# Kernel tuning notes

Measured on AMD Instinct MI355X. Metric: run time of the kernel, lower is better.

Reference implementation:

```python
import jax, jax.numpy as jnp
import numpy as np


def setup_inputs() -> dict:
    key = jax.random.key(0)
    k1, k2 = jax.random.split(key)
    B, D, K = 8192, 4096, 16
    x = jax.random.normal(k1, (B, D), dtype=jnp.float32)
    # kaiming_uniform_(a=sqrt(5)) on [K, D]: bound = sqrt(6/((1+5)*fan_in)) = 1/sqrt(D)
    bound = 1.0 / np.sqrt(D)
    w = jax.random.uniform(k2, (K, D), dtype=jnp.float32, minval=-bound, maxval=bound)
    return {"x": x, "w": w}


def reference(x, w):
    # z[b,d] = x[b,d] * (1 + sum_{i=1..k} w[i-1,d] * x[b,(d+i) mod D])
    k = w.shape[0]
    acc = jnp.ones_like(x)
    for i in range(1, k + 1):
        acc = acc + w[i - 1][None, :] * jnp.roll(x, -i, axis=1)
    return x * acc
```

## Files before the change

### kernel.cpp

```cpp
#include <hip/hip_runtime.h>


#define D 4096
#define DG 1024
#define K 16
#define TPB 256
#define TILE_B 8
#define ROW_F4 260
#define ROW_F (ROW_F4 * 4)

__global__ __launch_bounds__(TPB) void quad_enhancer_kernel(
    const float* __restrict__ x, const float* __restrict__ w,
    float* __restrict__ out) {
  __shared__ float lds[TILE_B * ROW_F];

  const int tid = threadIdx.x;
  const int cg0 = blockIdx.x * TPB;
  const int cg = cg0 + tid;
  const int b0 = blockIdx.y * TILE_B;

  const float4* x4 = (const float4*)x;

#pragma unroll
  for (int r = 0; r < TILE_B; ++r) {
    const float4* gptr = &x4[(size_t)(b0 + r) * DG + cg];
    float* lptr = &lds[r * ROW_F + tid * 4];
    __builtin_amdgcn_global_load_lds(
        (const __attribute__((address_space(1))) void*)gptr,
        (__attribute__((address_space(3))) void*)lptr, 16, 0, 0);
  }
  float4 halo;
  int hr = 0, hj = 0;
  if (tid < TILE_B * 4) {
    hr = tid >> 2;
    hj = tid & 3;
    halo = x4[(size_t)(b0 + hr) * DG + ((cg0 + 256 + hj) & (DG - 1))];
  }

  const float4* w4 = (const float4*)w;
  float4 wv[K];
#pragma unroll
  for (int i = 0; i < K; ++i) wv[i] = w4[i * DG + cg];

  if (tid < TILE_B * 4) {
    *(float4*)&lds[hr * ROW_F + (256 + hj) * 4] = halo;
  }
  __syncthreads();

  float4* out4 = (float4*)out;
#pragma unroll 2
  for (int r = 0; r < TILE_B; ++r) {
    const float4* lrow = (const float4*)&lds[r * ROW_F];
    float xs[20];
#pragma unroll
    for (int j = 0; j < 5; ++j) {
      float4 v = lrow[tid + j];
      xs[4 * j + 0] = v.x;
      xs[4 * j + 1] = v.y;
      xs[4 * j + 2] = v.z;
      xs[4 * j + 3] = v.w;
    }
    float ax = 1.0f, ay = 1.0f, az = 1.0f, aw = 1.0f;
#pragma unroll
    for (int i = 0; i < K; ++i) {
      ax = fmaf(wv[i].x, xs[i + 1], ax);
      ay = fmaf(wv[i].y, xs[i + 2], ay);
      az = fmaf(wv[i].z, xs[i + 3], az);
      aw = fmaf(wv[i].w, xs[i + 4], aw);
    }
    float4 o;
    o.x = xs[0] * ax;
    o.y = xs[1] * ay;
    o.z = xs[2] * az;
    o.w = xs[3] * aw;
    out4[(size_t)(b0 + r) * DG + cg] = o;
  }
}

extern "C" void kernel_launch(void* const* d_in, const int* in_sizes, int n_in,
                              void* d_out, int out_size, void* d_ws, size_t ws_size,
                              hipStream_t stream) {
  const float* x = (const float*)d_in[0];
  const float* w = (const float*)d_in[1];
  float* out = (float*)d_out;
  const int B = in_sizes[0] / D;

  dim3 grid(DG / TPB, B / TILE_B);
  quad_enhancer_kernel<<<grid, TPB, 0, stream>>>(x, w, out);
}
```

Baseline: 235.8 us.

## Replace LDS staging with direct register double-buffered global loads and nontemporal stores

Removes the shared-memory tile and barrier. Each thread now loads its own float4 plus the four neighbouring float4s straight from global memory, relying on the cache to serve the overlapping reads. Rows are processed in a two-buffer register pipeline over 16 rows per block, and outputs are written with nontemporal stores. This trades LDS traffic and synchronisation for five times as many global load instructions and more register pressure, and it halves the grid size.

```diff
diff --git a/kernel.cpp b/kernel.cpp
--- a/kernel.cpp
+++ b/kernel.cpp
@@ -5,60 +5,47 @@
 #define DG 1024
 #define K 16
 #define TPB 256
-#define TILE_B 8
-#define ROW_F4 260
-#define ROW_F (ROW_F4 * 4)
+#define RPB 16
+
+typedef float f32x4 __attribute__((ext_vector_type(4)));
 
 __global__ __launch_bounds__(TPB) void quad_enhancer_kernel(
     const float* __restrict__ x, const float* __restrict__ w,
     float* __restrict__ out) {
-  __shared__ float lds[TILE_B * ROW_F];
+  const int tid = threadIdx.x;
+  const int cg = blockIdx.x * TPB + tid;
+  const int b0 = blockIdx.y * RPB;
 
-  const int tid = threadIdx.x;
-  const int cg0 = blockIdx.x * TPB;
-  const int cg = cg0 + tid;
-  const int b0 = blockIdx.y * TILE_B;
+  const float4* __restrict__ x4 = (const float4*)x;
+  const float4* __restrict__ w4 = (const float4*)w;
+  f32x4* __restrict__ out4 = (f32x4*)out;
 
-  const float4* x4 = (const float4*)x;
+  const int g1 = (cg + 1) & (DG - 1);
+  const int g2 = (cg + 2) & (DG - 1);
+  const int g3 = (cg + 3) & (DG - 1);
+  const int g4 = (cg + 4) & (DG - 1);
 
-#pragma unroll
-  for (int r = 0; r < TILE_B; ++r) {
-    const float4* gptr = &x4[(size_t)(b0 + r) * DG + cg];
-    float* lptr = &lds[r * ROW_F + tid * 4];
-    __builtin_amdgcn_global_load_lds(
-        (const __attribute__((address_space(1))) void*)gptr,
-        (__attribute__((address_space(3))) void*)lptr, 16, 0, 0);
-  }
-  float4 halo;
-  int hr = 0, hj = 0;
-  if (tid < TILE_B * 4) {
-    hr = tid >> 2;
-    hj = tid & 3;
-    halo = x4[(size_t)(b0 + hr) * DG + ((cg0 + 256 + hj) & (DG - 1))];
-  }
-
-  const float4* w4 = (const float4*)w;
   float4 wv[K];
 #pragma unroll
   for (int i = 0; i < K; ++i) wv[i] = w4[i * DG + cg];
 
-  if (tid < TILE_B * 4) {
-    *(float4*)&lds[hr * ROW_F + (256 + hj) * 4] = halo;
-  }
-  __syncthreads();
+  auto loadrow = [&](int b, float4* buf) {
+    const float4* __restrict__ xr = x4 + (size_t)b * DG;
+    buf[0] = xr[cg];
+    buf[1] = xr[g1];
+    buf[2] = xr[g2];
+    buf[3] = xr[g3];
+    buf[4] = xr[g4];
+  };
 
-  float4* out4 = (float4*)out;
-#pragma unroll 2
-  for (int r = 0; r < TILE_B; ++r) {
-    const float4* lrow = (const float4*)&lds[r * ROW_F];
+  auto compute_store = [&](int b, const float4* buf) {
     float xs[20];
 #pragma unroll
     for (int j = 0; j < 5; ++j) {
-      float4 v = lrow[tid + j];
-      xs[4 * j + 0] = v.x;
-      xs[4 * j + 1] = v.y;
-      xs[4 * j + 2] = v.z;
-      xs[4 * j + 3] = v.w;
+      xs[4 * j + 0] = buf[j].x;
+      xs[4 * j + 1] = buf[j].y;
+      xs[4 * j + 2] = buf[j].z;
+      xs[4 * j + 3] = buf[j].w;
     }
     float ax = 1.0f, ay = 1.0f, az = 1.0f, aw = 1.0f;
 #pragma unroll
@@ -68,12 +55,22 @@
       az = fmaf(wv[i].z, xs[i + 3], az);
       aw = fmaf(wv[i].w, xs[i + 4], aw);
     }
-    float4 o;
+    f32x4 o;
     o.x = xs[0] * ax;
     o.y = xs[1] * ay;
     o.z = xs[2] * az;
     o.w = xs[3] * aw;
-    out4[(size_t)(b0 + r) * DG + cg] = o;
+    __builtin_nontemporal_store(o, &out4[(size_t)b * DG + cg]);
+  };
+
+  float4 bufA[5], bufB[5];
+  loadrow(b0, bufA);
+#pragma unroll 1
+  for (int r = 0; r < RPB; r += 2) {
+    loadrow(b0 + r + 1, bufB);
+    compute_store(b0 + r, bufA);
+    if (r + 2 < RPB) loadrow(b0 + r + 2, bufA);
+    compute_store(b0 + r + 1, bufB);
   }
 }
 
@@ -85,6 +82,6 @@
   float* out = (float*)d_out;
   const int B = in_sizes[0] / D;
 
-  dim3 grid(DG / TPB, B / TILE_B);
+  dim3 grid(DG / TPB, B / RPB);
   quad_enhancer_kernel<<<grid, TPB, 0, stream>>>(x, w, out);
 }
```

Result: slower. 256.4 us (+8.7%).

## Double-buffer LDS row tiles across a persistent row loop with nontemporal stores

Applied to the files above, without the earlier changes.

Each block now handles 32 rows as eight 4-row tiles. The next tile is loaded into a second LDS buffer with async global_load_lds while the current tile is computed, and w is loaded into registers once per block instead of once per 8 rows. Output uses nontemporal stores to reduce cache pollution. The trade-off is a grid four times smaller (1024 blocks), which leaves less parallelism for hiding latency, plus a per-tile barrier.

```diff
diff --git a/kernel.cpp b/kernel.cpp
--- a/kernel.cpp
+++ b/kernel.cpp
@@ -5,75 +5,103 @@
 #define DG 1024
 #define K 16
 #define TPB 256
-#define TILE_B 8
+#define TILE_B 4
+#define NT 8
 #define ROW_F4 260
 #define ROW_F (ROW_F4 * 4)
+#define BUF_F (TILE_B * ROW_F)
+
+typedef float f32x4 __attribute__((ext_vector_type(4)));
 
 __global__ __launch_bounds__(TPB) void quad_enhancer_kernel(
     const float* __restrict__ x, const float* __restrict__ w,
     float* __restrict__ out) {
-  __shared__ float lds[TILE_B * ROW_F];
+  __shared__ float lds[2 * BUF_F];
 
   const int tid = threadIdx.x;
   const int cg0 = blockIdx.x * TPB;
   const int cg = cg0 + tid;
-  const int b0 = blockIdx.y * TILE_B;
+  const int b0 = blockIdx.y * (TILE_B * NT);
 
-  const float4* x4 = (const float4*)x;
+  const float4* __restrict__ x4 = (const float4*)x;
+  const float4* __restrict__ w4 = (const float4*)w;
+  f32x4* __restrict__ o4 = (f32x4*)out;
 
+  const int hr = tid >> 2;
+  const int hj = tid & 3;
+  const int hg = (cg0 + 256 + hj) & (DG - 1);
+
+  auto stage = [&](int t, int q) {
 #pragma unroll
-  for (int r = 0; r < TILE_B; ++r) {
-    const float4* gptr = &x4[(size_t)(b0 + r) * DG + cg];
-    float* lptr = &lds[r * ROW_F + tid * 4];
-    __builtin_amdgcn_global_load_lds(
-        (const __attribute__((address_space(1))) void*)gptr,
-        (__attribute__((address_space(3))) void*)lptr, 16, 0, 0);
-  }
-  float4 halo;
-  int hr = 0, hj = 0;
-  if (tid < TILE_B * 4) {
-    hr = tid >> 2;
-    hj = tid & 3;
-    halo = x4[(size_t)(b0 + hr) * DG + ((cg0 + 256 + hj) & (DG - 1))];
-  }
+    for (int r = 0; r < TILE_B; ++r) {
+      const float4* gptr = &x4[(size_t)(b0 + t * TILE_B + r) * DG + cg];
+      float* lptr = &lds[q * BUF_F + r * ROW_F + tid * 4];
+      __builtin_amdgcn_global_load_lds(
+          (const __attribute__((address_space(1))) void*)gptr,
+          (__attribute__((address_space(3))) void*)lptr, 16, 0, 0);
+    }
+  };
 
-  const float4* w4 = (const float4*)w;
+  stage(0, 0);
+
   float4 wv[K];
 #pragma unroll
   for (int i = 0; i < K; ++i) wv[i] = w4[i * DG + cg];
 
   if (tid < TILE_B * 4) {
-    *(float4*)&lds[hr * ROW_F + (256 + hj) * 4] = halo;
+    float4 h0 = x4[(size_t)(b0 + hr) * DG + hg];
+    *(float4*)&lds[hr * ROW_F + (256 + hj) * 4] = h0;
   }
   __syncthreads();
 
-  float4* out4 = (float4*)out;
+#pragma unroll 1
+  for (int t = 0; t < NT; ++t) {
+    const int p = t & 1;
+    const int q = p ^ 1;
+
+    float4 haloN;
+    if (t + 1 < NT) {
+      stage(t + 1, q);
+      if (tid < TILE_B * 4) {
+        haloN = x4[(size_t)(b0 + (t + 1) * TILE_B + hr) * DG + hg];
+      }
+    }
+
 #pragma unroll 2
-  for (int r = 0; r < TILE_B; ++r) {
-    const float4* lrow = (const float4*)&lds[r * ROW_F];
-    float xs[20];
+    for (int r = 0; r < TILE_B; ++r) {
+      const float4* lrow = (const float4*)&lds[p * BUF_F + r * ROW_F];
+      float xs[20];
 #pragma unroll
-    for (int j = 0; j < 5; ++j) {
-      float4 v = lrow[tid + j];
-      xs[4 * j + 0] = v.x;
-      xs[4 * j + 1] = v.y;
-      xs[4 * j + 2] = v.z;
-      xs[4 * j + 3] = v.w;
+      for (int j = 0; j < 5; ++j) {
+        float4 v = lrow[tid + j];
+        xs[4 * j + 0] = v.x;
+        xs[4 * j + 1] = v.y;
+        xs[4 * j + 2] = v.z;
+        xs[4 * j + 3] = v.w;
+      }
+      float ax = 1.0f, ay = 1.0f, az = 1.0f, aw = 1.0f;
+#pragma unroll
+      for (int i = 0; i < K; ++i) {
+        ax = fmaf(wv[i].x, xs[i + 1], ax);
+        ay = fmaf(wv[i].y, xs[i + 2], ay);
+        az = fmaf(wv[i].z, xs[i + 3], az);
+        aw = fmaf(wv[i].w, xs[i + 4], aw);
+      }
+      f32x4 o;
+      o.x = xs[0] * ax;
+      o.y = xs[1] * ay;
+      o.z = xs[2] * az;
+      o.w = xs[3] * aw;
+      __builtin_nontemporal_store(
+          o, &o4[(size_t)(b0 + t * TILE_B + r) * DG + cg]);
     }
-    float ax = 1.0f, ay = 1.0f, az = 1.0f, aw = 1.0f;
-#pragma unroll
-    for (int i = 0; i < K; ++i) {
-      ax = fmaf(wv[i].x, xs[i + 1], ax);
-      ay = fmaf(wv[i].y, xs[i + 2], ay);
-      az = fmaf(wv[i].z, xs[i + 3], az);
-      aw = fmaf(wv[i].w, xs[i + 4], aw);
+
+    if (t + 1 < NT) {
+      if (tid < TILE_B * 4) {
+        *(float4*)&lds[q * BUF_F + hr * ROW_F + (256 + hj) * 4] = haloN;
+      }
+      __syncthreads();
     }
-    float4 o;
-    o.x = xs[0] * ax;
-    o.y = xs[1] * ay;
-    o.z = xs[2] * az;
-    o.w = xs[3] * aw;
-    out4[(size_t)(b0 + r) * DG + cg] = o;
   }
 }
 
@@ -85,6 +113,6 @@
   float* out = (float*)d_out;
   const int B = in_sizes[0] / D;
 
-  dim3 grid(DG / TPB, B / TILE_B);
+  dim3 grid(DG / TPB, B / (TILE_B * NT));
   quad_enhancer_kernel<<<grid, TPB, 0, stream>>>(x, w, out);
 }
```

Result: slower. 242.9 us (+3.0%).

## Double-buffer LDS row tiles with async loads across multiple tiles per block

Applied to the files above, without the earlier changes.

Each block now handles 32 rows as 8 tiles of 4 rows. The next tile is prefetched into a second LDS buffer with global_load_lds while the current tile is computed, and the halo is fetched asynchronously into its own LDS region. The weight registers are loaded once per block and reused across all 32 rows, so far fewer blocks reload weights. The cost is a 4x smaller grid with fewer resident waves, plus hand-written vmcnt waits that count outstanding stores as well as loads. That makes the synchronisation fragile.

```diff
diff --git a/kernel.cpp b/kernel.cpp
--- a/kernel.cpp
+++ b/kernel.cpp
@@ -5,75 +5,107 @@
 #define DG 1024
 #define K 16
 #define TPB 256
-#define TILE_B 8
-#define ROW_F4 260
-#define ROW_F (ROW_F4 * 4)
+#define TILE_B 4
+#define NT 8
+#define ROWS_PER_BLK (TILE_B * NT)
+#define BUF_F4 (TILE_B * 256)
+#define HALO_F4 64
+
+typedef float f32x4 __attribute__((ext_vector_type(4)));
 
 __global__ __launch_bounds__(TPB) void quad_enhancer_kernel(
     const float* __restrict__ x, const float* __restrict__ w,
     float* __restrict__ out) {
-  __shared__ float lds[TILE_B * ROW_F];
+  __shared__ float4 ldsbuf[2 * BUF_F4 + 2 * HALO_F4];
 
   const int tid = threadIdx.x;
+  const int lane = tid & 63;
   const int cg0 = blockIdx.x * TPB;
   const int cg = cg0 + tid;
-  const int b0 = blockIdx.y * TILE_B;
+  const int b0 = blockIdx.y * ROWS_PER_BLK;
 
-  const float4* x4 = (const float4*)x;
+  const float4* __restrict__ x4 = (const float4*)x;
+  const float4* __restrict__ w4 = (const float4*)w;
+  float4* __restrict__ o4 = (float4*)out;
 
+  float4* const buf0 = &ldsbuf[0];
+  float4* const buf1 = &ldsbuf[BUF_F4];
+  float4* const halo0 = &ldsbuf[2 * BUF_F4];
+  float4* const halo1 = &ldsbuf[2 * BUF_F4 + HALO_F4];
+
+  const int hrow = lane >> 2;
+  const int hcol = (cg0 + 256 + (lane & 3)) & (DG - 1);
+
+  auto stage = [&](int t, float4* buf, float4* halo) {
+    const int bb = b0 + t * TILE_B;
 #pragma unroll
-  for (int r = 0; r < TILE_B; ++r) {
-    const float4* gptr = &x4[(size_t)(b0 + r) * DG + cg];
-    float* lptr = &lds[r * ROW_F + tid * 4];
+    for (int r = 0; r < TILE_B; ++r) {
+      const float4* gptr = &x4[(size_t)(bb + r) * DG + cg];
+      __builtin_amdgcn_global_load_lds(
+          (const __attribute__((address_space(1))) void*)gptr,
+          (__attribute__((address_space(3))) void*)&buf[r * 256 + tid],
+          16, 0, 0);
+    }
+    const float4* hptr = (lane < 16) ? &x4[(size_t)(bb + hrow) * DG + hcol]
+                                     : &x4[(size_t)bb * DG + cg];
     __builtin_amdgcn_global_load_lds(
-        (const __attribute__((address_space(1))) void*)gptr,
-        (__attribute__((address_space(3))) void*)lptr, 16, 0, 0);
-  }
-  float4 halo;
-  int hr = 0, hj = 0;
-  if (tid < TILE_B * 4) {
-    hr = tid >> 2;
-    hj = tid & 3;
-    halo = x4[(size_t)(b0 + hr) * DG + ((cg0 + 256 + hj) & (DG - 1))];
-  }
+        (const __attribute__((address_space(1))) void*)hptr,
+        (__attribute__((address_space(3))) void*)&halo[lane], 16, 0, 0);
+  };
 
-  const float4* w4 = (const float4*)w;
+  stage(0, buf0, halo0);
+
   float4 wv[K];
 #pragma unroll
   for (int i = 0; i < K; ++i) wv[i] = w4[i * DG + cg];
 
-  if (tid < TILE_B * 4) {
-    *(float4*)&lds[hr * ROW_F + (256 + hj) * 4] = halo;
-  }
-  __syncthreads();
+  asm volatile("s_waitcnt vmcnt(0)" ::: "memory");
 
-  float4* out4 = (float4*)out;
-#pragma unroll 2
-  for (int r = 0; r < TILE_B; ++r) {
-    const float4* lrow = (const float4*)&lds[r * ROW_F];
-    float xs[20];
-#pragma unroll
-    for (int j = 0; j < 5; ++j) {
-      float4 v = lrow[tid + j];
-      xs[4 * j + 0] = v.x;
-      xs[4 * j + 1] = v.y;
-      xs[4 * j + 2] = v.z;
-      xs[4 * j + 3] = v.w;
-    }
-    float ax = 1.0f, ay = 1.0f, az = 1.0f, aw = 1.0f;
+#pragma unroll 1
+  for (int t = 0; t < NT; ++t) {
+    asm volatile("s_waitcnt vmcnt(4)" ::: "memory");
+    __builtin_amdgcn_s_barrier();
+    asm volatile("" ::: "memory");
+
 #pragma unroll
     for (int i = 0; i < K; ++i) {
-      ax = fmaf(wv[i].x, xs[i + 1], ax);
-      ay = fmaf(wv[i].y, xs[i + 2], ay);
-      az = fmaf(wv[i].z, xs[i + 3], az);
-      aw = fmaf(wv[i].w, xs[i + 4], aw);
+      asm volatile("" : "+v"(wv[i].x), "+v"(wv[i].y), "+v"(wv[i].z),
+                        "+v"(wv[i].w));
     }
-    float4 o;
-    o.x = xs[0] * ax;
-    o.y = xs[1] * ay;
-    o.z = xs[2] * az;
-    o.w = xs[3] * aw;
-    out4[(size_t)(b0 + r) * DG + cg] = o;
+
+    float4* const bufp = (t & 1) ? buf1 : buf0;
+    float4* const halop = (t & 1) ? halo1 : halo0;
+    if (t + 1 < NT) stage(t + 1, (t & 1) ? buf0 : buf1,
+                          (t & 1) ? halo0 : halo1);
+
+#pragma unroll 2
+    for (int r = 0; r < TILE_B; ++r) {
+      float xs[20];
+#pragma unroll
+      for (int j = 0; j < 5; ++j) {
+        const int g = tid + j;
+        float4 v = (g < 256) ? bufp[r * 256 + g]
+                             : halop[(r << 2) + (g - 256)];
+        xs[4 * j + 0] = v.x;
+        xs[4 * j + 1] = v.y;
+        xs[4 * j + 2] = v.z;
+        xs[4 * j + 3] = v.w;
+      }
+      float ax = 1.0f, ay = 1.0f, az = 1.0f, aw = 1.0f;
+#pragma unroll
+      for (int i = 0; i < K; ++i) {
+        ax = fmaf(wv[i].x, xs[i + 1], ax);
+        ay = fmaf(wv[i].y, xs[i + 2], ay);
+        az = fmaf(wv[i].z, xs[i + 3], az);
+        aw = fmaf(wv[i].w, xs[i + 4], aw);
+      }
+      float4 o;
+      o.x = xs[0] * ax;
+      o.y = xs[1] * ay;
+      o.z = xs[2] * az;
+      o.w = xs[3] * aw;
+      o4[(size_t)(b0 + t * TILE_B + r) * DG + cg] = o;
+    }
   }
 }
 
@@ -85,6 +117,6 @@
   float* out = (float*)d_out;
   const int B = in_sizes[0] / D;
 
-  dim3 grid(DG / TPB, B / TILE_B);
+  dim3 grid(DG / TPB, B / ROWS_PER_BLK);
   quad_enhancer_kernel<<<grid, TPB, 0, stream>>>(x, w, out);
 }
```

Result: slower. 248.8 us (+5.5%).
